# Kernel optimization log

Measured on AMD Instinct MI355X. Metric: run time of the kernel, lower is better.

## Reference

```python
import jax, jax.numpy as jnp
import numpy as np

B, N, D, H, L = 4, 1024, 256, 4, 2  # batch, nodes, mem_dim, heads, gcn sublayers
DK = D // H


def setup_inputs() -> dict:
    key = jax.random.key(0)
    ks = jax.random.split(key, 12)
    s = 0.05  # weight scale
    return {
        "gcn_inputs": jax.random.normal(ks[0], (B, N, D), jnp.float32),
        "rel_embs": jax.random.normal(ks[1], (B, N, D), jnp.float32),
        "adj": jax.random.randint(ks[2], (B, N, N), 0, 2, jnp.int32),
        "mask": jnp.zeros((B, 1, N), jnp.int32),  # 0 == valid token in this code's convention
        "W_Q": jax.random.normal(ks[3], (2 * D, D), jnp.float32) * s,
        "b_Q": jnp.zeros((D,), jnp.float32),
        "W_K": jax.random.normal(ks[4], (D, D), jnp.float32) * s,
        "b_K": jnp.zeros((D,), jnp.float32),
        "W_gcn": jax.random.normal(ks[5], (H * L, D, D), jnp.float32) * s,
        "b_gcn": jnp.zeros((H * L, D), jnp.float32),
        "W_out": jax.random.normal(ks[6], (D * H * L, D), jnp.float32) * s,
        "b_out": jnp.zeros((D,), jnp.float32),
    }


def _zscore_attn(scores, m, adj):
    """Faithful port of stdzscore + threshold + weightsoftmax chain.
    scores: [B,H,N,N]; m: bool [B,1,1,N] True=valid; adj: int [B,N,N]."""
    mf = m.astype(scores.dtype)
    # mymean (dim=[-1]): count from mask squeezed over dim -2 -> [B,1], +1e-4
    cnt_mean = mf[:, :, 0, :].sum(-1)[..., None] + 1e-4  # [B,1,1]
    ds = jnp.where(m, scores, 0.0).sum(-1)               # [B,H,N]
    mean = ds / cnt_mean                                  # [B,H,N]
    # mystd (dim=[-1]): count from full mask summed over -1 -> [B,1,1], +1e-4
    cnt_std = mf.sum(-1) + 1e-4                           # [B,1,1]
    sdata = jnp.where(m, (scores - mean[..., None]) ** 2, 0.0).sum(-1)
    std = jnp.sqrt(sdata / cnt_std + 1e-10)               # [B,H,N]
    z = (scores - mean[..., None]) / (std[..., None] + 1e-4)
    z = jnp.where(m, z, 0.0)
    thresh = z < 0
    s2 = jnp.where(thresh, -1e9, z)
    s2 = jnp.where(m, s2, -1e9)
    # weightsoftmax: stable exp, multiply by adjacency, mask, renormalize
    e = jnp.exp(s2 - s2.max(-1, keepdims=True))
    e = e * adj.astype(scores.dtype)[:, None]             # [B,H,N,N]
    e = jnp.where(m, e, 0.0) + 1e-10
    w = e / e.sum(-1, keepdims=True)
    w = jnp.where(m, w, 0.0)
    kill = (~m) | thresh | (adj == 0)[:, None]
    return jnp.where(kill, 0.0, w)


def reference(gcn_inputs, rel_embs, adj, mask, W_Q, b_Q, W_K, b_K, W_gcn, b_gcn, W_out, b_out):
    m = (mask == 0)[:, :, None, :]  # [B,1,1,N] True = valid
    # MultiHeadAttention: q from cat(query, rel), k from query
    q = (jnp.concatenate([gcn_inputs, rel_embs], -1) @ W_Q + b_Q)
    q = q.reshape(B, N, H, DK).transpose(0, 2, 1, 3)      # [B,H,N,DK]
    k = (gcn_inputs @ W_K + b_K).reshape(B, N, H, DK).transpose(0, 2, 1, 3)
    scores = jnp.einsum('bhnd,bhmd->bhnm', q, k)
    p_attn = _zscore_attn(scores, m, adj)                 # [B,H,N,N]
    # MultiGraphConvLayer (dropout = identity at inference)
    head_outs = []
    for i in range(H):
        a = p_attn[:, i]                                  # [B,N,N]
        denom = a.sum(2, keepdims=True) + 1.0             # [B,N,1]
        outputs = gcn_inputs
        layer_outs = []
        for l in range(L):
            idx = i * L + l
            Ax = jnp.einsum('bnm,bmd->bnd', a, outputs)
            # Linear applied to BOTH Ax and outputs (bias added twice, as in source)
            AxW = (Ax @ W_gcn[idx] + b_gcn[idx]) + (outputs @ W_gcn[idx] + b_gcn[idx])
            outputs = jax.nn.relu(AxW / denom)
            layer_outs.append(outputs)
        head_outs.append(jnp.concatenate(layer_outs, -1))  # [B,N,D*L]
    final = jnp.concatenate(head_outs, -1)                 # [B,N,D*L*H]
    return gcn_inputs + final @ W_out + b_out
```

## Files before the change

kernel.cpp:

```cpp
#include <hip/hip_runtime.h>
#include <math.h>

typedef unsigned short u16;
typedef __attribute__((ext_vector_type(8))) short short8;
typedef __attribute__((ext_vector_type(4))) float floatx4;

#define LDS_P 72

__device__ __forceinline__ float bf2f(u16 u) {
  union { unsigned int i; float f; } v; v.i = ((unsigned int)u) << 16; return v.f;
}
__device__ __forceinline__ u16 f2bf(float f) {
  union { float f; unsigned int i; } v; v.f = f;
  unsigned int x = v.i;
  return (u16)((x + 0x7FFFu + ((x >> 16) & 1u)) >> 16);
}

__device__ __forceinline__ void mfma_loop(const u16* __restrict__ A, int lda,
                                          const u16* __restrict__ Bt, int ldb,
                                          int K, u16* As, u16* Bs,
                                          floatx4 acc[2][2], int tid) {
  int lane = tid & 63;
  int wm = ((tid >> 6) & 1) << 5, wn = ((tid >> 6) >> 1) << 5;
  int lr = lane & 15, lq8 = (lane >> 4) << 3;
  int r0 = tid >> 3, c8 = (tid & 7) << 3;

  const u16* pA0 = A + (long long)r0 * lda + c8;
  const u16* pA1 = A + (long long)(r0 + 32) * lda + c8;
  const u16* pB0 = Bt + (long long)r0 * ldb + c8;
  const u16* pB1 = Bt + (long long)(r0 + 32) * ldb + c8;
  float4 a0 = *reinterpret_cast<const float4*>(pA0);
  float4 a1 = *reinterpret_cast<const float4*>(pA1);
  float4 b0 = *reinterpret_cast<const float4*>(pB0);
  float4 b1 = *reinterpret_cast<const float4*>(pB1);
  *reinterpret_cast<float4*>(As + r0 * LDS_P + c8) = a0;
  *reinterpret_cast<float4*>(As + (r0 + 32) * LDS_P + c8) = a1;
  *reinterpret_cast<float4*>(Bs + r0 * LDS_P + c8) = b0;
  *reinterpret_cast<float4*>(Bs + (r0 + 32) * LDS_P + c8) = b1;
  __syncthreads();

  int nslab = K >> 6;
  for (int s = 0; s < nslab; ++s) {
    const u16* Ac = As + (s & 1) * 4608;
    const u16* Bc = Bs + (s & 1) * 4608;
    if (s + 1 < nslab) {
      int off = (s + 1) << 6;
      a0 = *reinterpret_cast<const float4*>(pA0 + off);
      a1 = *reinterpret_cast<const float4*>(pA1 + off);
      b0 = *reinterpret_cast<const float4*>(pB0 + off);
      b1 = *reinterpret_cast<const float4*>(pB1 + off);
    }
#pragma unroll
    for (int kc = 0; kc < 64; kc += 32) {
      short8 fa0 = *reinterpret_cast<const short8*>(Ac + (wm + lr) * LDS_P + kc + lq8);
      short8 fa1 = *reinterpret_cast<const short8*>(Ac + (wm + 16 + lr) * LDS_P + kc + lq8);
      short8 fb0 = *reinterpret_cast<const short8*>(Bc + (wn + lr) * LDS_P + kc + lq8);
      short8 fb1 = *reinterpret_cast<const short8*>(Bc + (wn + 16 + lr) * LDS_P + kc + lq8);
      acc[0][0] = __builtin_amdgcn_mfma_f32_16x16x32_bf16(fa0, fb0, acc[0][0], 0, 0, 0);
      acc[0][1] = __builtin_amdgcn_mfma_f32_16x16x32_bf16(fa0, fb1, acc[0][1], 0, 0, 0);
      acc[1][0] = __builtin_amdgcn_mfma_f32_16x16x32_bf16(fa1, fb0, acc[1][0], 0, 0, 0);
      acc[1][1] = __builtin_amdgcn_mfma_f32_16x16x32_bf16(fa1, fb1, acc[1][1], 0, 0, 0);
    }
    if (s + 1 < nslab) {
      u16* An = As + ((s + 1) & 1) * 4608;
      u16* Bn = Bs + ((s + 1) & 1) * 4608;
      *reinterpret_cast<float4*>(An + r0 * LDS_P + c8) = a0;
      *reinterpret_cast<float4*>(An + (r0 + 32) * LDS_P + c8) = a1;
      *reinterpret_cast<float4*>(Bn + r0 * LDS_P + c8) = b0;
      *reinterpret_cast<float4*>(Bn + (r0 + 32) * LDS_P + c8) = b1;
    }
    __syncthreads();
  }
}

#define EPI_SETUP                                                     \
  int lane = threadIdx.x & 63;                                        \
  int wm = ((threadIdx.x >> 6) & 1) << 5,                             \
      wn = ((threadIdx.x >> 6) >> 1) << 5;                            \
  int lr = lane & 15, lq4 = (lane >> 4) << 2;

__global__ __launch_bounds__(256) void proj2_k(
    const u16* __restrict__ A, const u16* __restrict__ WQT,
    const u16* __restrict__ WKT, const float* __restrict__ b_Q,
    const float* __restrict__ b_K, u16* __restrict__ qbf,
    u16* __restrict__ kbf) {
  __shared__ u16 As[2 * 64 * LDS_P], Bs[2 * 64 * LDS_P];
  int z = blockIdx.z;
  int m0 = blockIdx.y << 6, n0 = blockIdx.x << 6;
  int K = z ? 256 : 512, ldb = z ? 256 : 512;
  const u16* Bt = z ? WKT : WQT;
  const float* bias = z ? b_K : b_Q;
  u16* C = z ? kbf : qbf;
  floatx4 acc[2][2] = {};
  mfma_loop(A + (long long)m0 * 512, 512, Bt + (long long)n0 * ldb, ldb, K, As, Bs,
            acc, threadIdx.x);
  EPI_SETUP
#pragma unroll
  for (int ti = 0; ti < 2; ++ti)
#pragma unroll
    for (int tj = 0; tj < 2; ++tj)
#pragma unroll
      for (int r = 0; r < 4; ++r) {
        int row = m0 + wm + ti * 16 + lq4 + r;
        int col = n0 + wn + tj * 16 + lr;
        C[(long long)row * 256 + col] = f2bf(acc[ti][tj][r] + bias[col]);
      }
}

__global__ __launch_bounds__(256) void mscore_k(
    const u16* __restrict__ q, const u16* __restrict__ kb,
    u16* __restrict__ sc) {
  __shared__ u16 As[2 * 64 * LDS_P], Bs[2 * 64 * LDS_P];
  int z = blockIdx.z;
  int b = z & 3, h = z >> 2;
  int m0 = blockIdx.y << 6, n0 = blockIdx.x << 6;
  const u16* Ab = q + b * 262144 + h * 64;
  const u16* Bb = kb + b * 262144 + h * 64;
  floatx4 acc[2][2] = {};
  mfma_loop(Ab + (long long)m0 * 256, 256, Bb + (long long)n0 * 256, 256, 64, As, Bs,
            acc, threadIdx.x);
  u16* Cb = sc + ((long long)z << 20);
  EPI_SETUP
#pragma unroll
  for (int ti = 0; ti < 2; ++ti)
#pragma unroll
    for (int tj = 0; tj < 2; ++tj)
#pragma unroll
      for (int r = 0; r < 4; ++r) {
        int row = m0 + wm + ti * 16 + lq4 + r;
        int col = n0 + wn + tj * 16 + lr;
        Cb[(long long)row * 1024 + col] = f2bf(acc[ti][tj][r]);
      }
}

__device__ __forceinline__ float wred_sum(float v) {
#pragma unroll
  for (int m = 32; m > 0; m >>= 1) v += __shfl_xor(v, m, 64);
  return v;
}
__device__ __forceinline__ void wred_sum2(float& a, float& b) {
#pragma unroll
  for (int m = 32; m > 0; m >>= 1) {
    float ta = __shfl_xor(a, m, 64);
    float tb = __shfl_xor(b, m, 64);
    a += ta; b += tb;
  }
}
__device__ __forceinline__ float wred_max(float v) {
#pragma unroll
  for (int m = 32; m > 0; m >>= 1) v = fmaxf(v, __shfl_xor(v, m, 64));
  return v;
}

__global__ __launch_bounds__(256) void zscore_w(
    const u16* __restrict__ sc, const int* __restrict__ adj,
    const int* __restrict__ mask, u16* __restrict__ wout,
    float* __restrict__ denh) {
  int wv = threadIdx.x >> 6, lane = threadIdx.x & 63;
  int row = (blockIdx.x << 2) + wv;
  int b = row >> 10, n = row & 1023;
  int e0 = lane << 4;
  const int* arow = adj + ((long long)row << 10) + e0;
  const int* mrow = mask + (b << 10) + e0;

  unsigned int vbits = 0, abits = 0;
#pragma unroll
  for (int q = 0; q < 4; ++q) {
    int4 a4 = *reinterpret_cast<const int4*>(arow + (q << 2));
    int4 m4 = *reinterpret_cast<const int4*>(mrow + (q << 2));
    vbits |= (unsigned)(m4.x == 0) << (q * 4);
    vbits |= (unsigned)(m4.y == 0) << (q * 4 + 1);
    vbits |= (unsigned)(m4.z == 0) << (q * 4 + 2);
    vbits |= (unsigned)(m4.w == 0) << (q * 4 + 3);
    abits |= (unsigned)(a4.x != 0) << (q * 4);
    abits |= (unsigned)(a4.y != 0) << (q * 4 + 1);
    abits |= (unsigned)(a4.z != 0) << (q * 4 + 2);
    abits |= (unsigned)(a4.w != 0) << (q * 4 + 3);
  }
  float cnt = wred_sum((float)__popc(vbits));
  float cnteff = cnt + 0.0001f;

  for (int h = 0; h < 4; ++h) {
    int z = (h << 2) + b;
    const u16* srow = sc + ((long long)z << 20) + ((long long)n << 10) + e0;
    float s[16];
#pragma unroll
    for (int q = 0; q < 2; ++q) {
      uint4 u = *reinterpret_cast<const uint4*>(srow + (q << 3));
      unsigned int uu[4] = {u.x, u.y, u.z, u.w};
#pragma unroll
      for (int t = 0; t < 4; ++t) {
        union { unsigned int i; float f; } lo, hi;
        lo.i = uu[t] << 16;
        hi.i = uu[t] & 0xffff0000u;
        s[q * 8 + t * 2] = lo.f;
        s[q * 8 + t * 2 + 1] = hi.f;
      }
    }
    float suml = 0.f, sql = 0.f;
#pragma unroll
    for (int u = 0; u < 16; ++u)
      if ((vbits >> u) & 1) { suml += s[u]; sql += s[u] * s[u]; }
    wred_sum2(suml, sql);
    float mean = suml / cnteff;
    float sdata = sql - 2.f * mean * suml + cnt * mean * mean;
    float stdv = sqrtf(fmaxf(sdata, 0.f) / cnteff + 1e-10f);
    float inv = 1.f / (stdv + 0.0001f);

    float maxl = -1e9f;
#pragma unroll
    for (int u = 0; u < 16; ++u) {
      float zz = (s[u] - mean) * inv;
      int vv = (vbits >> u) & 1;
      zz = vv ? zz : 0.f;
      s[u] = zz;
      if (vv && zz >= 0.f) maxl = fmaxf(maxl, zz);
    }
    float rowmax = wred_max(maxl);

    float e[16], el = 0.f;
#pragma unroll
    for (int u = 0; u < 16; ++u) {
      int vv = (vbits >> u) & 1, aa = (abits >> u) & 1;
      float ev = (vv && aa && (s[u] >= 0.f)) ? expf(s[u] - rowmax) : 0.f;
      e[u] = ev + 1e-10f;
      el += e[u];
    }
    float esum = wred_sum(el);
    float rinv = 1.f / esum;

    float wl = 0.f;
    unsigned int wo[8];
#pragma unroll
    for (int u = 0; u < 16; u += 2) {
      int s0 = ((vbits >> u) & 1) && ((abits >> u) & 1) && (s[u] >= 0.f);
      int s1 = ((vbits >> (u + 1)) & 1) && ((abits >> (u + 1)) & 1) && (s[u + 1] >= 0.f);
      float w0 = s0 ? e[u] * rinv : 0.f;
      float w1 = s1 ? e[u + 1] * rinv : 0.f;
      wl += w0 + w1;
      wo[u >> 1] = (unsigned)f2bf(w0) | ((unsigned)f2bf(w1) << 16);
    }
    float wsum = wred_sum(wl);

    u16* orow = wout + ((size_t)z << 20) + ((size_t)n << 10) + e0;
    reinterpret_cast<uint4*>(orow)[0] = make_uint4(wo[0], wo[1], wo[2], wo[3]);
    reinterpret_cast<uint4*>(orow)[1] = make_uint4(wo[4], wo[5], wo[6], wo[7]);
    if (lane == 0) denh[(z << 10) + n] = wsum + 1.0f;
  }
}

__global__ __launch_bounds__(512) void gcn_k(
    const u16* __restrict__ wght, const u16* __restrict__ srcT, int zmaskB,
    const u16* __restrict__ addsrc, int ldadd, long long sAdd, int hmul,
    const u16* __restrict__ WgT_all, const float* __restrict__ bg_all,
    const float* __restrict__ den, int l,
    u16* __restrict__ obT, u16* __restrict__ fin) {
  __shared__ u16 lds[53760];
  u16* As0 = lds;
  u16* As1 = lds + 4608;
  u16* Bs0 = lds + 9216;
  u16* Bs1 = lds + 27648;
  u16* Ts = lds;
  u16* Ws0 = lds + 16896;
  u16* Ws1 = lds + 35328;
  int tid = threadIdx.x;
  int m0 = blockIdx.x << 6;
  int z = blockIdx.y;
  int lane = tid & 63, w = tid >> 6;
  int wm = (w & 1) << 5, wn = (w >> 1) << 6;
  int lr = lane & 15, lq8 = (lane >> 4) << 3, lq4 = (lane >> 4) << 2;

  const u16* Aw = wght + ((long long)z << 20) + (long long)m0 * 1024;
  const u16* Bt = srcT + (long long)(z & zmaskB) * 262144;
  const u16* addb = addsrc + (long long)(z & 3) * sAdd + (z >> 2) * hmul;
  int idx2 = (z >> 2) * 2 + l;
  const u16* Wg = WgT_all + (long long)idx2 * 65536;

  floatx4 acc[2][4] = {};
  int rA = tid >> 3, cA = (tid & 7) << 3;
  int rowB[4], colB[4];
#pragma unroll
  for (int j = 0; j < 4; ++j) {
    int id = tid + (j << 9);
    rowB[j] = id >> 3; colB[j] = (id & 7) << 3;
  }

  float4 pa, pb[4];
  pa = *reinterpret_cast<const float4*>(Aw + (long long)rA * 1024 + cA);
#pragma unroll
  for (int j = 0; j < 4; ++j)
    pb[j] = *reinterpret_cast<const float4*>(Bt + (long long)rowB[j] * 1024 + colB[j]);
  *reinterpret_cast<float4*>(As0 + rA * 72 + cA) = pa;
#pragma unroll
  for (int j = 0; j < 4; ++j)
    *reinterpret_cast<float4*>(Bs0 + rowB[j] * 72 + colB[j]) = pb[j];
  __syncthreads();

  for (int s = 0; s < 16; ++s) {
    const u16* Ac = (s & 1) ? As1 : As0;
    const u16* Bc = (s & 1) ? Bs1 : Bs0;
    if (s < 15) {
      int off = (s + 1) << 6;
      pa = *reinterpret_cast<const float4*>(Aw + (long long)rA * 1024 + off + cA);
#pragma unroll
      for (int j = 0; j < 4; ++j)
        pb[j] = *reinterpret_cast<const float4*>(Bt + (long long)rowB[j] * 1024 + off + colB[j]);
    }
#pragma unroll
    for (int kc = 0; kc < 64; kc += 32) {
      short8 a[2], b[4];
#pragma unroll
      for (int t = 0; t < 2; ++t)
        a[t] = *reinterpret_cast<const short8*>(Ac + (wm + t * 16 + lr) * 72 + kc + lq8);
#pragma unroll
      for (int t = 0; t < 4; ++t)
        b[t] = *reinterpret_cast<const short8*>(Bc + (wn + t * 16 + lr) * 72 + kc + lq8);
#pragma unroll
      for (int ti = 0; ti < 2; ++ti)
#pragma unroll
        for (int tj = 0; tj < 4; ++tj)
          acc[ti][tj] =
              __builtin_amdgcn_mfma_f32_16x16x32_bf16(a[ti], b[tj], acc[ti][tj], 0, 0, 0);
    }
    if (s < 15) {
      u16* An = (s & 1) ? As0 : As1;
      u16* Bn = (s & 1) ? Bs0 : Bs1;
      *reinterpret_cast<float4*>(An + rA * 72 + cA) = pa;
#pragma unroll
      for (int j = 0; j < 4; ++j)
        *reinterpret_cast<float4*>(Bn + rowB[j] * 72 + colB[j]) = pb[j];
    }
    __syncthreads();
  }

#pragma unroll
  for (int ti = 0; ti < 2; ++ti)
#pragma unroll
    for (int tj = 0; tj < 4; ++tj)
#pragma unroll
      for (int r = 0; r < 4; ++r) {
        int row = wm + ti * 16 + lq4 + r;
        int col = wn + tj * 16 + lr;
        float v = acc[ti][tj][r] + bf2f(addb[(long long)(m0 + row) * ldadd + col]);
        Ts[row * 264 + col] = f2bf(v);
        acc[ti][tj][r] = 0.f;
      }
  float4 pw[4];
#pragma unroll
  for (int j = 0; j < 4; ++j)
    pw[j] = *reinterpret_cast<const float4*>(Wg + (long long)rowB[j] * 256 + colB[j]);
#pragma unroll
  for (int j = 0; j < 4; ++j)
    *reinterpret_cast<float4*>(Ws0 + rowB[j] * 72 + colB[j]) = pw[j];
  __syncthreads();

  for (int s = 0; s < 4; ++s) {
    const u16* Wc = (s & 1) ? Ws1 : Ws0;
    int kc0 = s << 6;
    if (s < 3) {
      int off = (s + 1) << 6;
#pragma unroll
      for (int j = 0; j < 4; ++j)
        pw[j] = *reinterpret_cast<const float4*>(Wg + (long long)rowB[j] * 256 + off + colB[j]);
    }
#pragma unroll
    for (int kc = 0; kc < 64; kc += 32) {
      short8 a[2], b[4];
#pragma unroll
      for (int t = 0; t < 2; ++t)
        a[t] = *reinterpret_cast<const short8*>(Ts + (wm + t * 16 + lr) * 264 + kc0 + kc + lq8);
#pragma unroll
      for (int t = 0; t < 4; ++t)
        b[t] = *reinterpret_cast<const short8*>(Wc + (wn + t * 16 + lr) * 72 + kc + lq8);
#pragma unroll
      for (int ti = 0; ti < 2; ++ti)
#pragma unroll
        for (int tj = 0; tj < 4; ++tj)
          acc[ti][tj] =
              __builtin_amdgcn_mfma_f32_16x16x32_bf16(a[ti], b[tj], acc[ti][tj], 0, 0, 0);
    }
    if (s < 3) {
      u16* Wn = (s & 1) ? Ws0 : Ws1;
#pragma unroll
      for (int j = 0; j < 4; ++j)
        *reinterpret_cast<float4*>(Wn + rowB[j] * 72 + colB[j]) = pw[j];
    }
    __syncthreads();
  }

  const float* bb = bg_all + idx2 * 256;
  const float* dn = den + (z << 10);
  long long finbase = (long long)(z & 3) * 2097152 + idx2 * 256;
#pragma unroll
  for (int ti = 0; ti < 2; ++ti) {
    int row = m0 + wm + ti * 16 + lq4;
#pragma unroll
    for (int tj = 0; tj < 4; ++tj) {
      int col = wn + tj * 16 + lr;
      u16 bv4[4];
#pragma unroll
      for (int r = 0; r < 4; ++r) {
        float v = (acc[ti][tj][r] + 2.f * bb[col]) / dn[row + r];
        v = fmaxf(v, 0.f);
        bv4[r] = f2bf(v);
        fin[finbase + (long long)(row + r) * 2048 + col] = bv4[r];
      }
      if (obT) {
        ushort4 t4 = {bv4[0], bv4[1], bv4[2], bv4[3]};
        *reinterpret_cast<ushort4*>(obT + ((long long)z << 18) +
                                    (long long)col * 1024 + row) = t4;
      }
    }
  }
}

__global__ __launch_bounds__(512) void mfinal_k(
    const u16* __restrict__ fin, const u16* __restrict__ WoT,
    const float* __restrict__ X, const float* __restrict__ bias,
    float* __restrict__ out) {
  __shared__ u16 lds[36864];
  u16* As0 = lds;
  u16* As1 = lds + 4608;
  u16* Bs0 = lds + 9216;
  u16* Bs1 = lds + 13824;
  int tid = threadIdx.x;
  int m0 = blockIdx.y << 6, n0 = blockIdx.x << 6;
  int lane = tid & 63, w = tid >> 6;
  int wm = (w & 3) << 4, wn = (w >> 2) << 5;
  int lr = lane & 15, lq8 = (lane >> 4) << 3, lq4 = (lane >> 4) << 2;

  const u16* Ab = fin + (long long)m0 * 2048;
  const u16* Bb = WoT + (long long)n0 * 2048;
  int r0 = tid >> 3, c8 = (tid & 7) << 3;

  floatx4 acc[2] = {};
  float4 pa = *reinterpret_cast<const float4*>(Ab + (long long)r0 * 2048 + c8);
  float4 pb = *reinterpret_cast<const float4*>(Bb + (long long)r0 * 2048 + c8);
  *reinterpret_cast<float4*>(As0 + r0 * 72 + c8) = pa;
  *reinterpret_cast<float4*>(Bs0 + r0 * 72 + c8) = pb;
  __syncthreads();

  for (int s = 0; s < 32; ++s) {
    const u16* Ac = (s & 1) ? As1 : As0;
    const u16* Bc = (s & 1) ? Bs1 : Bs0;
    if (s < 31) {
      int off = (s + 1) << 6;
      pa = *reinterpret_cast<const float4*>(Ab + (long long)r0 * 2048 + off + c8);
      pb = *reinterpret_cast<const float4*>(Bb + (long long)r0 * 2048 + off + c8);
    }
#pragma unroll
    for (int kc = 0; kc < 64; kc += 32) {
      short8 a = *reinterpret_cast<const short8*>(Ac + (wm + lr) * 72 + kc + lq8);
      short8 b0 = *reinterpret_cast<const short8*>(Bc + (wn + lr) * 72 + kc + lq8);
      short8 b1 = *reinterpret_cast<const short8*>(Bc + (wn + 16 + lr) * 72 + kc + lq8);
      acc[0] = __builtin_amdgcn_mfma_f32_16x16x32_bf16(a, b0, acc[0], 0, 0, 0);
      acc[1] = __builtin_amdgcn_mfma_f32_16x16x32_bf16(a, b1, acc[1], 0, 0, 0);
    }
    if (s < 31) {
      u16* An = (s & 1) ? As0 : As1;
      u16* Bn = (s & 1) ? Bs0 : Bs1;
      *reinterpret_cast<float4*>(An + r0 * 72 + c8) = pa;
      *reinterpret_cast<float4*>(Bn + r0 * 72 + c8) = pb;
    }
    __syncthreads();
  }

#pragma unroll
  for (int tj = 0; tj < 2; ++tj)
#pragma unroll
    for (int r = 0; r < 4; ++r) {
      int row = m0 + wm + lq4 + r;
      int col = n0 + wn + tj * 16 + lr;
      out[(long long)row * 256 + col] =
          acc[tj][r] + bias[col] + X[(long long)row * 256 + col];
    }
}

__global__ __launch_bounds__(256) void prep_k(
    const float* __restrict__ X, const float* __restrict__ R,
    const float* __restrict__ W_Q, const float* __restrict__ W_K,
    const float* __restrict__ W_gcn, const float* __restrict__ W_out,
    u16* __restrict__ A, u16* __restrict__ XT, u16* __restrict__ WQT,
    u16* __restrict__ WKT, u16* __restrict__ WgT, u16* __restrict__ WoT) {
  int bi = blockIdx.x;
  int tid = threadIdx.x;
  if (bi < 560) {
    __shared__ u16 tile[64 * LDS_P];
    const float* S;
    u16* D;
    int I, ti, tj;
    if (bi < 256) {
      int zz = bi >> 6, rem = bi & 63;
      ti = rem >> 2; tj = rem & 3; I = 1024;
      S = X + zz * 262144; D = XT + zz * 262144;
    } else if (bi < 288) {
      int t = bi - 256; ti = t >> 2; tj = t & 3; I = 512;
      S = W_Q; D = WQT;
    } else if (bi < 304) {
      int t = bi - 288; ti = t >> 2; tj = t & 3; I = 256;
      S = W_K; D = WKT;
    } else if (bi < 432) {
      int t = bi - 304; int zz = t >> 4, rem = t & 15;
      ti = rem >> 2; tj = rem & 3; I = 256;
      S = W_gcn + zz * 65536; D = WgT + zz * 65536;
    } else {
      int t = bi - 432; ti = t >> 2; tj = t & 3; I = 2048;
      S = W_out; D = WoT;
    }
    int rr = tid >> 4, cc = (tid & 15) << 2;
#pragma unroll
    for (int q = 0; q < 4; ++q) {
      int r = rr + (q << 4);
      float4 v = *reinterpret_cast<const float4*>(S + (long long)(ti * 64 + r) * 256 +
                                                  tj * 64 + cc);
      ushort4 h = {f2bf(v.x), f2bf(v.y), f2bf(v.z), f2bf(v.w)};
      *reinterpret_cast<ushort4*>(tile + r * LDS_P + cc) = h;
    }
    __syncthreads();
    int jl = tid >> 2, il = (tid & 3) << 4;
    u16 vals[16];
#pragma unroll
    for (int u = 0; u < 16; ++u) vals[u] = tile[(il + u) * LDS_P + jl];
    u16* dp = D + (long long)(tj * 64 + jl) * I + ti * 64 + il;
    reinterpret_cast<uint4*>(dp)[0] = *reinterpret_cast<uint4*>(vals);
    reinterpret_cast<uint4*>(dp)[1] = *reinterpret_cast<uint4*>(vals + 8);
  } else {
    int gid = (bi - 560) * 256 + tid;
    int col = gid & 511, row = gid >> 9;
    float v = (col < 256) ? X[row * 256 + col] : R[row * 256 + col - 256];
    A[gid] = f2bf(v);
  }
}

extern "C" void kernel_launch(void* const* d_in, const int* in_sizes, int n_in,
                              void* d_out, int out_size, void* d_ws, size_t ws_size,
                              hipStream_t stream) {
  const float* X = (const float*)d_in[0];
  const float* R = (const float*)d_in[1];
  const int* adj = (const int*)d_in[2];
  const int* mask = (const int*)d_in[3];
  const float* W_Q = (const float*)d_in[4];
  const float* b_Q = (const float*)d_in[5];
  const float* W_K = (const float*)d_in[6];
  const float* b_K = (const float*)d_in[7];
  const float* W_gcn = (const float*)d_in[8];
  const float* b_gcn = (const float*)d_in[9];
  const float* W_out = (const float*)d_in[10];
  const float* b_out = (const float*)d_in[11];
  float* out = (float*)d_out;

  u16* wsu = (u16*)d_ws;
  u16* A_qk = wsu;
  u16* qbf  = A_qk + (2u << 20);
  u16* kbf  = qbf + (1u << 20);
  u16* XT   = kbf + (1u << 20);
  u16* WQT  = XT + (1u << 20);
  u16* WKT  = WQT + (1u << 17);
  u16* WgT  = WKT + (1u << 16);
  u16* WoT  = WgT + (1u << 19);
  u16* obT  = WoT + (1u << 19);
  u16* finb = obT + (4u << 20);
  u16* wght = finb + (8u << 20);
  float* den = (float*)(wght + (16u << 20));
  u16* sc = (u16*)(den + (1 << 14));

  prep_k<<<8752, 256, 0, stream>>>(X, R, W_Q, W_K, W_gcn, W_out,
                                   A_qk, XT, WQT, WKT, WgT, WoT);

  proj2_k<<<dim3(4, 64, 2), 256, 0, stream>>>(A_qk, WQT, WKT, b_Q, b_K, qbf, kbf);

  mscore_k<<<dim3(16, 16, 16), 256, 0, stream>>>(qbf, kbf, sc);
  zscore_w<<<1024, 256, 0, stream>>>(sc, adj, mask, wght, den);

  gcn_k<<<dim3(16, 16), 512, 0, stream>>>(wght, XT, 3, A_qk, 512, 524288LL, 0,
                                          WgT, b_gcn, den, 0, obT, finb);
  gcn_k<<<dim3(16, 16), 512, 0, stream>>>(wght, obT, 15, finb, 2048, 2097152LL, 512,
                                          WgT, b_gcn, den, 1, nullptr, finb);

  mfinal_k<<<dim3(4, 64), 512, 0, stream>>>(finb, WoT, X, b_out, out);
}
```

Measured before the change: 210.9 us.

## Fuse score GEMM with z-score attention weighting in one kernel

Replaces the separate score-matrix GEMM and z-score/softmax kernels with a single kernel. Each block computes a 16-row slab of scores for all 1024 columns per head into LDS using MFMA, then runs the z-score, threshold and adjacency-weighted softmax directly from LDS. This removes the bf16 score matrix round trip through global memory and one launch. In exchange there are only 256 blocks with heavy LDS use, and K tiles are reloaded per block without double buffering, so parallelism and K reuse drop.

```diff
diff --git a/kernel.cpp b/kernel.cpp
--- a/kernel.cpp
+++ b/kernel.cpp
@@ -107,32 +107,6 @@
       }
 }
 
-__global__ __launch_bounds__(256) void mscore_k(
-    const u16* __restrict__ q, const u16* __restrict__ kb,
-    u16* __restrict__ sc) {
-  __shared__ u16 As[2 * 64 * LDS_P], Bs[2 * 64 * LDS_P];
-  int z = blockIdx.z;
-  int b = z & 3, h = z >> 2;
-  int m0 = blockIdx.y << 6, n0 = blockIdx.x << 6;
-  const u16* Ab = q + b * 262144 + h * 64;
-  const u16* Bb = kb + b * 262144 + h * 64;
-  floatx4 acc[2][2] = {};
-  mfma_loop(Ab + (long long)m0 * 256, 256, Bb + (long long)n0 * 256, 256, 64, As, Bs,
-            acc, threadIdx.x);
-  u16* Cb = sc + ((long long)z << 20);
-  EPI_SETUP
-#pragma unroll
-  for (int ti = 0; ti < 2; ++ti)
-#pragma unroll
-    for (int tj = 0; tj < 2; ++tj)
-#pragma unroll
-      for (int r = 0; r < 4; ++r) {
-        int row = m0 + wm + ti * 16 + lq4 + r;
-        int col = n0 + wn + tj * 16 + lr;
-        Cb[(long long)row * 1024 + col] = f2bf(acc[ti][tj][r]);
-      }
-}
-
 __device__ __forceinline__ float wred_sum(float v) {
 #pragma unroll
   for (int m = 32; m > 0; m >>= 1) v += __shfl_xor(v, m, 64);
@@ -152,100 +126,159 @@
   return v;
 }
 
-__global__ __launch_bounds__(256) void zscore_w(
-    const u16* __restrict__ sc, const int* __restrict__ adj,
-    const int* __restrict__ mask, u16* __restrict__ wout,
-    float* __restrict__ denh) {
-  int wv = threadIdx.x >> 6, lane = threadIdx.x & 63;
-  int row = (blockIdx.x << 2) + wv;
-  int b = row >> 10, n = row & 1023;
+__global__ __launch_bounds__(512) void score_z_k(
+    const u16* __restrict__ qbf, const u16* __restrict__ kbf,
+    const int* __restrict__ adj, const int* __restrict__ mask,
+    u16* __restrict__ wout, float* __restrict__ denh) {
+  __shared__ u16 lds[58624];
+  u16* Ssc = lds;
+  u16* Ash = lds + 16512;
+  u16* Bsh = lds + 17664;
+  int tid = threadIdx.x;
+  int lane = tid & 63, w = tid >> 6;
+  int lr = lane & 15, lq8 = (lane >> 4) << 3, lq4 = (lane >> 4) << 2;
+  int b = blockIdx.x >> 6;
+  int n0 = (blockIdx.x & 63) << 4;
+  int wn = w << 7;
+
+  const u16* qb = qbf + (long long)(b * 1024 + n0) * 256;
+  const u16* kb = kbf + (long long)b * 262144;
+  u16* Bw = Bsh + w * 5120;
+
   int e0 = lane << 4;
-  const int* arow = adj + ((long long)row << 10) + e0;
   const int* mrow = mask + (b << 10) + e0;
-
-  unsigned int vbits = 0, abits = 0;
+  unsigned int vbits = 0;
 #pragma unroll
   for (int q = 0; q < 4; ++q) {
-    int4 a4 = *reinterpret_cast<const int4*>(arow + (q << 2));
     int4 m4 = *reinterpret_cast<const int4*>(mrow + (q << 2));
     vbits |= (unsigned)(m4.x == 0) << (q * 4);
     vbits |= (unsigned)(m4.y == 0) << (q * 4 + 1);
     vbits |= (unsigned)(m4.z == 0) << (q * 4 + 2);
     vbits |= (unsigned)(m4.w == 0) << (q * 4 + 3);
-    abits |= (unsigned)(a4.x != 0) << (q * 4);
-    abits |= (unsigned)(a4.y != 0) << (q * 4 + 1);
-    abits |= (unsigned)(a4.z != 0) << (q * 4 + 2);
-    abits |= (unsigned)(a4.w != 0) << (q * 4 + 3);
+  }
+  unsigned int ab2[2];
+#pragma unroll
+  for (int rr = 0; rr < 2; ++rr) {
+    int n = n0 + (w << 1) + rr;
+    const int* arow = adj + (((long long)(b * 1024 + n)) << 10) + e0;
+    unsigned int abits = 0;
+#pragma unroll
+    for (int q = 0; q < 4; ++q) {
+      int4 a4 = *reinterpret_cast<const int4*>(arow + (q << 2));
+      abits |= (unsigned)(a4.x != 0) << (q * 4);
+      abits |= (unsigned)(a4.y != 0) << (q * 4 + 1);
+      abits |= (unsigned)(a4.z != 0) << (q * 4 + 2);
+      abits |= (unsigned)(a4.w != 0) << (q * 4 + 3);
+    }
+    ab2[rr] = abits;
   }
   float cnt = wred_sum((float)__popc(vbits));
   float cnteff = cnt + 0.0001f;
 
   for (int h = 0; h < 4; ++h) {
-    int z = (h << 2) + b;
-    const u16* srow = sc + ((long long)z << 20) + ((long long)n << 10) + e0;
-    float s[16];
-#pragma unroll
-    for (int q = 0; q < 2; ++q) {
-      uint4 u = *reinterpret_cast<const uint4*>(srow + (q << 3));
-      unsigned int uu[4] = {u.x, u.y, u.z, u.w};
-#pragma unroll
-      for (int t = 0; t < 4; ++t) {
-        union { unsigned int i; float f; } lo, hi;
-        lo.i = uu[t] << 16;
-        hi.i = uu[t] & 0xffff0000u;
-        s[q * 8 + t * 2] = lo.f;
-        s[q * 8 + t * 2 + 1] = hi.f;
-      }
-    }
-    float suml = 0.f, sql = 0.f;
-#pragma unroll
-    for (int u = 0; u < 16; ++u)
-      if ((vbits >> u) & 1) { suml += s[u]; sql += s[u] * s[u]; }
-    wred_sum2(suml, sql);
-    float mean = suml / cnteff;
-    float sdata = sql - 2.f * mean * suml + cnt * mean * mean;
-    float stdv = sqrtf(fmaxf(sdata, 0.f) / cnteff + 1e-10f);
-    float inv = 1.f / (stdv + 0.0001f);
-
-    float maxl = -1e9f;
-#pragma unroll
-    for (int u = 0; u < 16; ++u) {
-      float zz = (s[u] - mean) * inv;
-      int vv = (vbits >> u) & 1;
-      zz = vv ? zz : 0.f;
-      s[u] = zz;
-      if (vv && zz >= 0.f) maxl = fmaxf(maxl, zz);
-    }
-    float rowmax = wred_max(maxl);
-
-    float e[16], el = 0.f;
-#pragma unroll
-    for (int u = 0; u < 16; ++u) {
-      int vv = (vbits >> u) & 1, aa = (abits >> u) & 1;
-      float ev = (vv && aa && (s[u] >= 0.f)) ? expf(s[u] - rowmax) : 0.f;
-      e[u] = ev + 1e-10f;
-      el += e[u];
-    }
-    float esum = wred_sum(el);
-    float rinv = 1.f / esum;
-
-    float wl = 0.f;
-    unsigned int wo[8];
-#pragma unroll
-    for (int u = 0; u < 16; u += 2) {
-      int s0 = ((vbits >> u) & 1) && ((abits >> u) & 1) && (s[u] >= 0.f);
-      int s1 = ((vbits >> (u + 1)) & 1) && ((abits >> (u + 1)) & 1) && (s[u + 1] >= 0.f);
-      float w0 = s0 ? e[u] * rinv : 0.f;
-      float w1 = s1 ? e[u + 1] * rinv : 0.f;
-      wl += w0 + w1;
-      wo[u >> 1] = (unsigned)f2bf(w0) | ((unsigned)f2bf(w1) << 16);
-    }
-    float wsum = wred_sum(wl);
-
-    u16* orow = wout + ((size_t)z << 20) + ((size_t)n << 10) + e0;
-    reinterpret_cast<uint4*>(orow)[0] = make_uint4(wo[0], wo[1], wo[2], wo[3]);
-    reinterpret_cast<uint4*>(orow)[1] = make_uint4(wo[4], wo[5], wo[6], wo[7]);
-    if (lane == 0) denh[(z << 10) + n] = wsum + 1.0f;
+    if (tid < 128) {
+      int rrow = tid >> 3, c8 = (tid & 7) << 3;
+      *reinterpret_cast<uint4*>(Ash + rrow * 72 + c8) =
+          *reinterpret_cast<const uint4*>(qb + (long long)rrow * 256 + h * 64 + c8);
+    }
+    __syncthreads();
+
+    floatx4 acc[8] = {};
+#pragma unroll
+    for (int kh = 0; kh < 64; kh += 32) {
+#pragma unroll
+      for (int j = 0; j < 4; ++j) {
+        int t = (lane >> 1) + (j << 5);
+        int f = (lane & 1) << 4;
+        const u16* src = kb + (long long)(wn + t) * 256 + h * 64 + kh + f;
+        u16* dst = Bw + t * 40 + f;
+        *reinterpret_cast<uint4*>(dst) = *reinterpret_cast<const uint4*>(src);
+        *reinterpret_cast<uint4*>(dst + 8) = *reinterpret_cast<const uint4*>(src + 8);
+      }
+      short8 a = *reinterpret_cast<const short8*>(Ash + lr * 72 + kh + lq8);
+#pragma unroll
+      for (int tj = 0; tj < 8; ++tj) {
+        short8 bf = *reinterpret_cast<const short8*>(Bw + (tj * 16 + lr) * 40 + lq8);
+        acc[tj] = __builtin_amdgcn_mfma_f32_16x16x32_bf16(a, bf, acc[tj], 0, 0, 0);
+      }
+    }
+#pragma unroll
+    for (int tj = 0; tj < 8; ++tj)
+#pragma unroll
+      for (int r = 0; r < 4; ++r)
+        Ssc[(lq4 + r) * 1032 + wn + tj * 16 + lr] = f2bf(acc[tj][r]);
+    __syncthreads();
+
+    for (int rr = 0; rr < 2; ++rr) {
+      int row = (w << 1) + rr;
+      int n = n0 + row;
+      unsigned int abits = ab2[rr];
+      const u16* srow = Ssc + row * 1032 + e0;
+      float s[16];
+      {
+        uint4 u0 = *reinterpret_cast<const uint4*>(srow);
+        uint4 u1 = *reinterpret_cast<const uint4*>(srow + 8);
+        unsigned int uu[8] = {u0.x, u0.y, u0.z, u0.w, u1.x, u1.y, u1.z, u1.w};
+#pragma unroll
+        for (int t = 0; t < 8; ++t) {
+          union { unsigned int i; float f; } lo, hi;
+          lo.i = uu[t] << 16;
+          hi.i = uu[t] & 0xffff0000u;
+          s[t * 2] = lo.f;
+          s[t * 2 + 1] = hi.f;
+        }
+      }
+      float suml = 0.f, sql = 0.f;
+#pragma unroll
+      for (int u = 0; u < 16; ++u)
+        if ((vbits >> u) & 1) { suml += s[u]; sql += s[u] * s[u]; }
+      wred_sum2(suml, sql);
+      float mean = suml / cnteff;
+      float sdata = sql - 2.f * mean * suml + cnt * mean * mean;
+      float stdv = sqrtf(fmaxf(sdata, 0.f) / cnteff + 1e-10f);
+      float inv = 1.f / (stdv + 0.0001f);
+
+      float maxl = -1e9f;
+#pragma unroll
+      for (int u = 0; u < 16; ++u) {
+        float zz = (s[u] - mean) * inv;
+        int vv = (vbits >> u) & 1;
+        zz = vv ? zz : 0.f;
+        s[u] = zz;
+        if (vv && zz >= 0.f) maxl = fmaxf(maxl, zz);
+      }
+      float rowmax = wred_max(maxl);
+
+      float e[16], el = 0.f;
+#pragma unroll
+      for (int u = 0; u < 16; ++u) {
+        int vv = (vbits >> u) & 1, aa = (abits >> u) & 1;
+        float ev = (vv && aa && (s[u] >= 0.f)) ? expf(s[u] - rowmax) : 0.f;
+        e[u] = ev + 1e-10f;
+        el += e[u];
+      }
+      float esum = wred_sum(el);
+      float rinv = 1.f / esum;
+
+      float wl = 0.f;
+      unsigned int wo[8];
+#pragma unroll
+      for (int u = 0; u < 16; u += 2) {
+        int s0 = ((vbits >> u) & 1) && ((abits >> u) & 1) && (s[u] >= 0.f);
+        int s1 = ((vbits >> (u + 1)) & 1) && ((abits >> (u + 1)) & 1) && (s[u + 1] >= 0.f);
+        float w0 = s0 ? e[u] * rinv : 0.f;
+        float w1 = s1 ? e[u + 1] * rinv : 0.f;
+        wl += w0 + w1;
+        wo[u >> 1] = (unsigned)f2bf(w0) | ((unsigned)f2bf(w1) << 16);
+      }
+      float wsum = wred_sum(wl);
+
+      int z = (h << 2) + b;
+      u16* orow = wout + ((size_t)z << 20) + ((size_t)n << 10) + e0;
+      reinterpret_cast<uint4*>(orow)[0] = make_uint4(wo[0], wo[1], wo[2], wo[3]);
+      reinterpret_cast<uint4*>(orow)[1] = make_uint4(wo[4], wo[5], wo[6], wo[7]);
+      if (lane == 0) denh[(z << 10) + n] = wsum + 1.0f;
+    }
   }
 }
 
@@ -562,15 +595,13 @@
   u16* finb = obT + (4u << 20);
   u16* wght = finb + (8u << 20);
   float* den = (float*)(wght + (16u << 20));
-  u16* sc = (u16*)(den + (1 << 14));
 
   prep_k<<<8752, 256, 0, stream>>>(X, R, W_Q, W_K, W_gcn, W_out,
                                    A_qk, XT, WQT, WKT, WgT, WoT);
 
   proj2_k<<<dim3(4, 64, 2), 256, 0, stream>>>(A_qk, WQT, WKT, b_Q, b_K, qbf, kbf);
 
-  mscore_k<<<dim3(16, 16, 16), 256, 0, stream>>>(qbf, kbf, sc);
-  zscore_w<<<1024, 256, 0, stream>>>(sc, adj, mask, wght, den);
+  score_z_k<<<256, 512, 0, stream>>>(qbf, kbf, adj, mask, wght, den);
 
   gcn_k<<<dim3(16, 16), 512, 0, stream>>>(wght, XT, 3, A_qk, 512, 524288LL, 0,
                                           WgT, b_gcn, den, 0, obT, finb);
```

Result: slower. 221.9 us (+5.2%).
